# Kernel tuning notes

Measured on AMD Instinct MI355X. Metric: run time of the kernel, lower is better.

Reference implementation:

```python
import jax, jax.numpy as jnp
import numpy as np

DIM = 4096
B, S = 4, 2048


def setup_inputs() -> dict:
    key = jax.random.key(0)
    ks = jax.random.split(key, 6)
    scale = 1.0 / np.sqrt(DIM)  # nn.Linear-style init scale
    return {
        "x": jax.random.normal(ks[0], (B, S, DIM), dtype=jnp.float32),
        "W1": jax.random.normal(ks[1], (DIM, DIM), dtype=jnp.float32) * scale,
        "W2": jax.random.normal(ks[2], (DIM, DIM), dtype=jnp.float32) * scale,
        "W3": jax.random.normal(ks[3], (DIM, DIM), dtype=jnp.float32) * scale,
        "W4": jax.random.normal(ks[4], (DIM, DIM), dtype=jnp.float32) * scale,
        "Wo": jax.random.normal(ks[5], (DIM, DIM), dtype=jnp.float32) * scale,
    }


def reference(x, W1, W2, W3, W4, Wo):
    # nn.Linear(bias=False): y = x @ W.T
    xA = jnp.einsum('bsd,ed->bse', x, W1)
    xB = jnp.einsum('bsd,ed->bse', x, W2)
    xC = jnp.einsum('bsd,ed->bse', x, W3)
    # xA^T @ xB over the sequence axis -> [B, dim, dim]
    sq = jnp.einsum('bsd,bse->bde', xA, xB)
    sq = jax.nn.softmax(sq, axis=-1)
    # xC @ sq -> [B, S, dim]
    xO = jnp.einsum('bsd,bde->bse', xC, sq)
    xO = jax.nn.softmax(xO, axis=-1)
    xO = jax.nn.silu(jnp.einsum('bsd,ed->bse', xO, W4))
    return jnp.einsum('bsd,ed->bse', x + xO, Wo)
```

## Files before the change

kernel.cpp:

```cpp
#include <hip/hip_runtime.h>
#include <hip/hip_bf16.h>
#include <stdint.h>

#define DIM 4096
#define NB 4
#define SEQ 2048

typedef __bf16 bf16_t;
typedef __bf16 bf16x8 __attribute__((ext_vector_type(8)));
typedef float f32x4 __attribute__((ext_vector_type(4)));

__device__ __forceinline__ uint16_t f2bf_u(float f) {
  union { float f; uint32_t u; } v; v.f = f;
  uint32_t r = v.u + 0x7FFFu + ((v.u >> 16) & 1u);
  return (uint16_t)(r >> 16);
}
__device__ __forceinline__ float bfu2f(uint32_t u) {
  union { uint32_t u; float f; } v; v.u = u << 16; return v.f;
}

__global__ __launch_bounds__(256) void cvt_f32_bf16_k(const float* __restrict__ in,
                                                      uint16_t* __restrict__ out, long n) {
  long i = ((long)blockIdx.x * 256 + threadIdx.x) * 8;
  long stride = (long)gridDim.x * 256 * 8;
  for (; i < n; i += stride) {
    float4 a = *(const float4*)(in + i);
    float4 b = *(const float4*)(in + i + 4);
    ushort4 o0 = make_ushort4(f2bf_u(a.x), f2bf_u(a.y), f2bf_u(a.z), f2bf_u(a.w));
    ushort4 o1 = make_ushort4(f2bf_u(b.x), f2bf_u(b.y), f2bf_u(b.z), f2bf_u(b.w));
    *(ushort4*)(out + i) = o0;
    *(ushort4*)(out + i + 4) = o1;
  }
}

__device__ __forceinline__ void gload16(const void* g, void* l) {
  __builtin_amdgcn_global_load_lds(
      (const __attribute__((address_space(1))) void*)g,
      (__attribute__((address_space(3))) void*)l,
      16, 0, 0);
}

#define BARX() do { asm volatile("" ::: "memory"); __builtin_amdgcn_s_barrier(); asm volatile("" ::: "memory"); } while (0)
#define VMW(n) asm volatile("s_waitcnt vmcnt(" #n ")" ::: "memory")

__device__ __forceinline__ void readA(bf16x8 (&fa)[4][2], const char* p, int c0, int c1) {
#pragma unroll
  for (int m = 0; m < 4; ++m) {
    fa[m][0] = *(const bf16x8*)(p + m * 2048 + c0);
    fa[m][1] = *(const bf16x8*)(p + m * 2048 + c1);
  }
}
__device__ __forceinline__ void readB(bf16x8 (&fb)[2][2], const char* p, int c0, int c1) {
#pragma unroll
  for (int n = 0; n < 2; ++n) {
    fb[n][0] = *(const bf16x8*)(p + n * 2048 + c0);
    fb[n][1] = *(const bf16x8*)(p + n * 2048 + c1);
  }
}
__device__ __forceinline__ void mmaQ(f32x4 (&acc)[4][2], const bf16x8 (&fa)[4][2],
                                     const bf16x8 (&fb)[2][2]) {
#pragma unroll
  for (int m = 0; m < 4; ++m)
#pragma unroll
    for (int n = 0; n < 2; ++n)
#pragma unroll
      for (int kk = 0; kk < 2; ++kk)
        acc[m][n] = __builtin_amdgcn_mfma_f32_16x16x32_bf16(fa[m][kk], fb[n][kk], acc[m][n], 0, 0, 0);
}
__device__ __forceinline__ void stageH(const bf16_t* gt, int soff, long rsk, char* lb, int t16) {
  gload16(gt + soff, lb + t16);
  gload16(gt + soff + rsk, lb + 8192 + t16);
}

#define PRIO1() __builtin_amdgcn_s_setprio(1)
#define PRIO0() __builtin_amdgcn_s_setprio(0)

template <int EPI>
__global__ __launch_bounds__(512, 2) void gemm256(
    const bf16_t* __restrict__ Abase, const bf16_t* __restrict__ Bbase,
    void* __restrict__ Cout, const float* __restrict__ Xadd,
    int M, int N, int K, long sA, long sB, long sC) {
  __shared__ char smem[131072];
  char* As = smem;
  char* Bs = smem + 65536;

  const int tid = threadIdx.x;
  const int lane = tid & 63;
  const int wave = tid >> 6;
  const int wm = wave >> 2;
  const int wn = wave & 3;
  const int lr = lane & 15;
  const int hi = lane >> 4;

  const int nwg = gridDim.x;
  int wg = blockIdx.x;
  if ((nwg & 7) == 0) wg = (wg & 7) * (nwg >> 3) + (wg >> 3);
  const int nbn = N >> 8;
  const int bm = wg / nbn, bn = wg % nbn;

  const bf16_t* A = Abase + (long)blockIdx.y * sA;
  const bf16_t* B = Bbase + (long)blockIdx.y * sB;
  const bf16_t* A0p = A + (long)(bm * 256) * K;
  const bf16_t* A1p = A0p + (long)128 * K;
  const bf16_t* B0p = B + (long)(bn * 256) * K;
  const bf16_t* B1p = B0p + (long)128 * K;
  const long rsk = (long)64 * K;

  const int t16 = tid * 16;
  const int lp = t16 ^ (((t16 >> 7) & 7) << 4);
  const int soff = (lp >> 7) * K + ((lp & 127) >> 1);

  const int swz = (lr & 7) << 4;
  const int c0 = (hi * 16) ^ swz;
  const int c1 = c0 ^ 64;
  const int aR = (wm * 64 + lr) * 128;
  const int bR = (wn * 32 + lr) * 128;

  f32x4 acc[2][2][4][2] = {};
  bf16x8 fa0[4][2], fa1[4][2], fb0[2][2], fb1[2][2];

  stageH(A0p, soff, rsk, As, t16);
  stageH(A1p, soff, rsk, As + 16384, t16);
  stageH(B0p, soff, rsk, Bs, t16);
  stageH(B1p, soff, rsk, Bs + 16384, t16);
  VMW(4);
  stageH(A0p + 64, soff, rsk, As + 32768, t16);
  stageH(A1p + 64, soff, rsk, As + 49152, t16);
  stageH(B0p + 64, soff, rsk, Bs + 32768, t16);
  VMW(6);
  BARX();

  const int NIT = K >> 7;
  for (int i = 0; i < NIT; ++i) {
    const bool last = (i == NIT - 1);
    const int k1 = (2 * i + 1) * 64;
    readA(fa0, As + aR, c0, c1);
    readB(fb0, Bs + bR, c0, c1);
    stageH(B1p + k1, soff, rsk, Bs + 49152, t16);
    BARX();
    PRIO1(); mmaQ(acc[0][0], fa0, fb0); PRIO0();
    BARX();
    readA(fa1, As + 16384 + aR, c0, c1);
    if (!last) stageH(A0p + k1 + 64, soff, rsk, As, t16);
    BARX();
    PRIO1(); mmaQ(acc[1][0], fa1, fb0); PRIO0();
    BARX();
    readB(fb1, Bs + 16384 + bR, c0, c1);
    if (!last) stageH(A1p + k1 + 64, soff, rsk, As + 16384, t16);
    BARX();
    PRIO1(); mmaQ(acc[0][1], fa0, fb1); PRIO0();
    BARX();
    if (!last) stageH(B0p + k1 + 64, soff, rsk, Bs, t16);
    BARX();
    PRIO1(); mmaQ(acc[1][1], fa1, fb1); PRIO0();
    if (last) { VMW(0); } else { VMW(6); }
    BARX();
    readA(fa0, As + 32768 + aR, c0, c1);
    readB(fb0, Bs + 32768 + bR, c0, c1);
    if (!last) stageH(B1p + k1 + 64, soff, rsk, Bs + 16384, t16);
    BARX();
    PRIO1(); mmaQ(acc[0][0], fa0, fb0); PRIO0();
    BARX();
    readA(fa1, As + 49152 + aR, c0, c1);
    if (!last) stageH(A0p + k1 + 128, soff, rsk, As + 32768, t16);
    BARX();
    PRIO1(); mmaQ(acc[1][0], fa1, fb0); PRIO0();
    BARX();
    readB(fb1, Bs + 49152 + bR, c0, c1);
    if (!last) stageH(A1p + k1 + 128, soff, rsk, As + 49152, t16);
    BARX();
    PRIO1(); mmaQ(acc[0][1], fa0, fb1); PRIO0();
    BARX();
    if (!last) stageH(B0p + k1 + 128, soff, rsk, Bs + 32768, t16);
    BARX();
    PRIO1(); mmaQ(acc[1][1], fa1, fb1); PRIO0();
    if (!last) VMW(6);
    BARX();
  }

  const long cb = (long)blockIdx.y * sC;
#pragma unroll
  for (int mh = 0; mh < 2; ++mh)
#pragma unroll
    for (int nh = 0; nh < 2; ++nh)
#pragma unroll
      for (int m = 0; m < 4; ++m)
#pragma unroll
        for (int n = 0; n < 2; ++n)
#pragma unroll
          for (int j = 0; j < 4; ++j) {
            const int row = bm * 256 + mh * 128 + wm * 64 + m * 16 + hi * 4 + j;
            const int col = bn * 256 + nh * 128 + wn * 32 + n * 16 + lr;
            const long idx = cb + (long)row * N + col;
            const float vv = acc[mh][nh][m][n][j];
            if constexpr (EPI == 0) {
              ((uint16_t*)Cout)[idx] = f2bf_u(vv);
            } else if constexpr (EPI == 1) {
              ((float*)Cout)[idx] = vv;
            } else {
              const float sl = vv / (1.f + __expf(-vv));
              ((uint16_t*)Cout)[idx] = f2bf_u(Xadd[idx] + sl);
            }
          }
}

__global__ __launch_bounds__(256) void rowstat4096_bf16(const uint16_t* __restrict__ in,
                                                        float2* __restrict__ stats) {
  const long row = blockIdx.x;
  const uint16_t* r = in + row * 4096;
  const int tid = threadIdx.x;
  uint32_t w[8];
  *(uint4*)(w) = *(const uint4*)(r + tid * 16);
  *(uint4*)(w + 4) = *(const uint4*)(r + tid * 16 + 8);
  float v[16];
#pragma unroll
  for (int j = 0; j < 8; ++j) {
    v[2 * j] = bfu2f(w[j] & 0xFFFFu);
    v[2 * j + 1] = bfu2f(w[j] >> 16);
  }
  float m = v[0];
#pragma unroll
  for (int j = 1; j < 16; ++j) m = fmaxf(m, v[j]);
#pragma unroll
  for (int o = 32; o; o >>= 1) m = fmaxf(m, __shfl_xor(m, o));
  __shared__ float red[8];
  if ((tid & 63) == 0) red[tid >> 6] = m;
  __syncthreads();
  m = fmaxf(fmaxf(red[0], red[1]), fmaxf(red[2], red[3]));
  float s = 0.f;
#pragma unroll
  for (int j = 0; j < 16; ++j) s += __expf(v[j] - m);
#pragma unroll
  for (int o = 32; o; o >>= 1) s += __shfl_xor(s, o);
  if ((tid & 63) == 0) red[4 + (tid >> 6)] = s;
  __syncthreads();
  if (tid == 0) {
    s = (red[4] + red[5]) + (red[6] + red[7]);
    stats[row] = make_float2(m, 1.f / s);
  }
}

__global__ __launch_bounds__(256) void transposeSM_bf16(const uint16_t* __restrict__ inB,
                                                        const float2* __restrict__ statsB,
                                                        uint16_t* __restrict__ outB) {
  const int b = blockIdx.z;
  const uint16_t* in = inB + (long)b * (4096L * 4096);
  const float2* stats = statsB + (long)b * 4096;
  uint16_t* out = outB + (long)b * (4096L * 4096);
  __shared__ uint16_t t[64][68];
  __shared__ float2 st[64];
  const int tid = threadIdx.x;
  const int bx = blockIdx.x, by = blockIdx.y;
  if (tid < 64) st[tid] = stats[by * 64 + tid];
  __syncthreads();
  const int tr = tid >> 4;
  const int tc4 = (tid & 15) * 4;
#pragma unroll
  for (int i = 0; i < 4; ++i) {
    const int r = tr + i * 16;
    const float2 ms = st[r];
    ushort4 u = *(const ushort4*)&in[(long)(by * 64 + r) * 4096 + bx * 64 + tc4];
    t[r][tc4 + 0] = f2bf_u(__expf(bfu2f(u.x) - ms.x) * ms.y);
    t[r][tc4 + 1] = f2bf_u(__expf(bfu2f(u.y) - ms.x) * ms.y);
    t[r][tc4 + 2] = f2bf_u(__expf(bfu2f(u.z) - ms.x) * ms.y);
    t[r][tc4 + 3] = f2bf_u(__expf(bfu2f(u.w) - ms.x) * ms.y);
  }
  __syncthreads();
#pragma unroll
  for (int i = 0; i < 4; ++i) {
    const int oc = tr + i * 16;
    ushort4 v = make_ushort4(t[tc4 + 0][oc], t[tc4 + 1][oc], t[tc4 + 2][oc], t[tc4 + 3][oc]);
    *(ushort4*)&out[(long)(bx * 64 + oc) * 4096 + by * 64 + tc4] = v;
  }
}

__global__ __launch_bounds__(256) void softmax_row4096_bf16(const uint16_t* __restrict__ in,
                                                            uint16_t* __restrict__ out) {
  const long row = blockIdx.x;
  const uint16_t* r = in + row * 4096;
  const int tid = threadIdx.x;
  uint32_t w[8];
  *(uint4*)(w) = *(const uint4*)(r + tid * 16);
  *(uint4*)(w + 4) = *(const uint4*)(r + tid * 16 + 8);
  float v[16];
#pragma unroll
  for (int j = 0; j < 8; ++j) {
    v[2 * j] = bfu2f(w[j] & 0xFFFFu);
    v[2 * j + 1] = bfu2f(w[j] >> 16);
  }
  float m = v[0];
#pragma unroll
  for (int j = 1; j < 16; ++j) m = fmaxf(m, v[j]);
#pragma unroll
  for (int o = 32; o; o >>= 1) m = fmaxf(m, __shfl_xor(m, o));
  __shared__ float red[8];
  if ((tid & 63) == 0) red[tid >> 6] = m;
  __syncthreads();
  m = fmaxf(fmaxf(red[0], red[1]), fmaxf(red[2], red[3]));
  float s = 0.f;
#pragma unroll
  for (int j = 0; j < 16; ++j) { v[j] = __expf(v[j] - m); s += v[j]; }
#pragma unroll
  for (int o = 32; o; o >>= 1) s += __shfl_xor(s, o);
  if ((tid & 63) == 0) red[4 + (tid >> 6)] = s;
  __syncthreads();
  s = (red[4] + red[5]) + (red[6] + red[7]);
  float inv = 1.f / s;
#pragma unroll
  for (int i = 0; i < 4; ++i) {
    ushort4 u = make_ushort4(f2bf_u(v[i * 4 + 0] * inv), f2bf_u(v[i * 4 + 1] * inv),
                             f2bf_u(v[i * 4 + 2] * inv), f2bf_u(v[i * 4 + 3] * inv));
    *(ushort4*)(out + row * 4096 + tid * 16 + i * 4) = u;
  }
}

extern "C" void kernel_launch(void* const* d_in, const int* in_sizes, int n_in,
                              void* d_out, int out_size, void* d_ws, size_t ws_size,
                              hipStream_t stream) {
  const float* x  = (const float*)d_in[0];
  const float* W1 = (const float*)d_in[1];
  const float* W2 = (const float*)d_in[2];
  const float* W3 = (const float*)d_in[3];
  const float* W4 = (const float*)d_in[4];
  const float* Wo = (const float*)d_in[5];

  char* ws = (char*)d_ws;
  const long SD  = (long)SEQ * DIM;
  const long BSD = (long)NB * SD;
  const long DD  = (long)DIM * DIM;

  bf16_t* xbf  = (bf16_t*)(ws + 0L);
  bf16_t* xW   = (bf16_t*)(ws + 67108864L);
  bf16_t* R3   = (bf16_t*)(ws + 201326592L);
  bf16_t* Wbf  = (bf16_t*)(ws + 268435456L);
  bf16_t* sqmT = (bf16_t*)(ws + 301989888L);
  float2* stats = (float2*)Wbf;
  (void)ws_size; (void)in_sizes; (void)n_in; (void)out_size;

  cvt_f32_bf16_k<<<2048, 256, 0, stream>>>(x, (uint16_t*)xbf, BSD);

  cvt_f32_bf16_k<<<2048, 256, 0, stream>>>(W1, (uint16_t*)R3, DD);
  cvt_f32_bf16_k<<<2048, 256, 0, stream>>>(W2, (uint16_t*)(R3 + DD), DD);
  gemm256<0><<<dim3(256, 4), 512, 0, stream>>>(R3, xbf, (void*)xW, nullptr,
                                               2 * DIM, SEQ, DIM, 0, SD, 2 * SD);

  gemm256<0><<<dim3(256, 4), 512, 0, stream>>>(xW, xW + SD, d_out, nullptr,
                                               DIM, DIM, SEQ, 2 * SD, 2 * SD, DD);
  rowstat4096_bf16<<<NB * DIM, 256, 0, stream>>>((const uint16_t*)d_out, stats);
  transposeSM_bf16<<<dim3(64, 64, 4), 256, 0, stream>>>((const uint16_t*)d_out, stats,
                                                        (uint16_t*)sqmT);

  cvt_f32_bf16_k<<<2048, 256, 0, stream>>>(W3, (uint16_t*)Wbf, DD);
  gemm256<0><<<dim3(512, 1), 512, 0, stream>>>(xbf, Wbf, (void*)R3, nullptr,
                                               NB * SEQ, DIM, DIM, 0, 0, 0);

  gemm256<0><<<dim3(128, 4), 512, 0, stream>>>(R3, sqmT, d_out, nullptr,
                                               SEQ, DIM, DIM, SD, DD, SD);
  softmax_row4096_bf16<<<NB * SEQ, 256, 0, stream>>>((const uint16_t*)d_out, (uint16_t*)xW);

  cvt_f32_bf16_k<<<2048, 256, 0, stream>>>(W4, (uint16_t*)Wbf, DD);
  gemm256<2><<<dim3(512, 1), 512, 0, stream>>>(xW, Wbf, (void*)xbf, x,
                                               NB * SEQ, DIM, DIM, 0, 0, 0);

  cvt_f32_bf16_k<<<2048, 256, 0, stream>>>(Wo, (uint16_t*)Wbf, DD);
  gemm256<1><<<dim3(512, 1), 512, 0, stream>>>(xbf, Wbf, d_out, nullptr,
                                               NB * SEQ, DIM, DIM, 0, 0, 0);
}
```

Baseline: 1.730 ms.

## Restructure GEMM main loop into a deeper software pipeline with fewer barriers

Rewrites the 256x256 bf16 GEMM main loop so each LDS fragment read is issued one step ahead of the MFMA that consumes it. The loop now uses one barrier per quarter-step instead of two, and keeps all eight half-tiles in flight using vmcnt(10) waits. The last-iteration branches are removed by wrapping prefetch offsets with a K mask, so the final iteration issues redundant loads from the start of K. This aims to overlap LDS reads, global-to-LDS loads and MFMA more tightly. The cost is extra wasted global traffic at the tail, and correctness depends on the reordered buffer reuse and waitcnt values being right.

```diff
diff --git a/kernel.cpp b/kernel.cpp
--- a/kernel.cpp
+++ b/kernel.cpp
@@ -42,6 +42,7 @@
 
 #define BARX() do { asm volatile("" ::: "memory"); __builtin_amdgcn_s_barrier(); asm volatile("" ::: "memory"); } while (0)
 #define VMW(n) asm volatile("s_waitcnt vmcnt(" #n ")" ::: "memory")
+#define LGKM(n) asm volatile("s_waitcnt lgkmcnt(" #n ")" ::: "memory")
 
 __device__ __forceinline__ void readA(bf16x8 (&fa)[4][2], const char* p, int c0, int c1) {
 #pragma unroll
@@ -120,62 +121,61 @@
   bf16x8 fa0[4][2], fa1[4][2], fb0[2][2], fb1[2][2];
 
   stageH(A0p, soff, rsk, As, t16);
-  stageH(A1p, soff, rsk, As + 16384, t16);
   stageH(B0p, soff, rsk, Bs, t16);
   stageH(B1p, soff, rsk, Bs + 16384, t16);
-  VMW(4);
+  stageH(A1p, soff, rsk, As + 16384, t16);
   stageH(A0p + 64, soff, rsk, As + 32768, t16);
+  stageH(B0p + 64, soff, rsk, Bs + 32768, t16);
+  stageH(B1p + 64, soff, rsk, Bs + 49152, t16);
   stageH(A1p + 64, soff, rsk, As + 49152, t16);
-  stageH(B0p + 64, soff, rsk, Bs + 32768, t16);
-  VMW(6);
+  VMW(12);
   BARX();
+  readA(fa0, As + aR, c0, c1);
+  readB(fb0, Bs + bR, c0, c1);
+  LGKM(0);
+  VMW(10);
+  BARX();
 
   const int NIT = K >> 7;
+  const int kmask = K - 1;
   for (int i = 0; i < NIT; ++i) {
-    const bool last = (i == NIT - 1);
-    const int k1 = (2 * i + 1) * 64;
+    const int k2 = (128 * i + 128) & kmask;
+    const int k3 = (128 * i + 192) & kmask;
+
+    readB(fb1, Bs + 16384 + bR, c0, c1);
+    stageH(A0p + k2, soff, rsk, As, t16);
+    PRIO1(); mmaQ(acc[0][0], fa0, fb0); PRIO0();
+    VMW(10); BARX();
+    readA(fa1, As + 16384 + aR, c0, c1);
+    stageH(B0p + k2, soff, rsk, Bs, t16);
+    PRIO1(); mmaQ(acc[0][1], fa0, fb1); PRIO0();
+    VMW(10); BARX();
+    readA(fa0, As + 32768 + aR, c0, c1);
+    stageH(B1p + k2, soff, rsk, Bs + 16384, t16);
+    PRIO1(); mmaQ(acc[1][1], fa1, fb1); PRIO0();
+    VMW(10); BARX();
+    PRIO1(); mmaQ(acc[1][0], fa1, fb0); PRIO0();
+    readB(fb0, Bs + 32768 + bR, c0, c1);
+    stageH(A1p + k2, soff, rsk, As + 16384, t16);
+    LGKM(4);
+    VMW(10); BARX();
+    readB(fb1, Bs + 49152 + bR, c0, c1);
+    stageH(A0p + k3, soff, rsk, As + 32768, t16);
+    PRIO1(); mmaQ(acc[0][0], fa0, fb0); PRIO0();
+    VMW(10); BARX();
+    readA(fa1, As + 49152 + aR, c0, c1);
+    stageH(B0p + k3, soff, rsk, Bs + 32768, t16);
+    PRIO1(); mmaQ(acc[0][1], fa0, fb1); PRIO0();
+    VMW(10); BARX();
     readA(fa0, As + aR, c0, c1);
+    stageH(B1p + k3, soff, rsk, Bs + 49152, t16);
+    PRIO1(); mmaQ(acc[1][1], fa1, fb1); PRIO0();
+    VMW(10); BARX();
+    PRIO1(); mmaQ(acc[1][0], fa1, fb0); PRIO0();
     readB(fb0, Bs + bR, c0, c1);
-    stageH(B1p + k1, soff, rsk, Bs + 49152, t16);
-    BARX();
-    PRIO1(); mmaQ(acc[0][0], fa0, fb0); PRIO0();
-    BARX();
-    readA(fa1, As + 16384 + aR, c0, c1);
-    if (!last) stageH(A0p + k1 + 64, soff, rsk, As, t16);
-    BARX();
-    PRIO1(); mmaQ(acc[1][0], fa1, fb0); PRIO0();
-    BARX();
-    readB(fb1, Bs + 16384 + bR, c0, c1);
-    if (!last) stageH(A1p + k1 + 64, soff, rsk, As + 16384, t16);
-    BARX();
-    PRIO1(); mmaQ(acc[0][1], fa0, fb1); PRIO0();
-    BARX();
-    if (!last) stageH(B0p + k1 + 64, soff, rsk, Bs, t16);
-    BARX();
-    PRIO1(); mmaQ(acc[1][1], fa1, fb1); PRIO0();
-    if (last) { VMW(0); } else { VMW(6); }
-    BARX();
-    readA(fa0, As + 32768 + aR, c0, c1);
-    readB(fb0, Bs + 32768 + bR, c0, c1);
-    if (!last) stageH(B1p + k1 + 64, soff, rsk, Bs + 16384, t16);
-    BARX();
-    PRIO1(); mmaQ(acc[0][0], fa0, fb0); PRIO0();
-    BARX();
-    readA(fa1, As + 49152 + aR, c0, c1);
-    if (!last) stageH(A0p + k1 + 128, soff, rsk, As + 32768, t16);
-    BARX();
-    PRIO1(); mmaQ(acc[1][0], fa1, fb0); PRIO0();
-    BARX();
-    readB(fb1, Bs + 49152 + bR, c0, c1);
-    if (!last) stageH(A1p + k1 + 128, soff, rsk, As + 49152, t16);
-    BARX();
-    PRIO1(); mmaQ(acc[0][1], fa0, fb1); PRIO0();
-    BARX();
-    if (!last) stageH(B0p + k1 + 128, soff, rsk, Bs + 32768, t16);
-    BARX();
-    PRIO1(); mmaQ(acc[1][1], fa1, fb1); PRIO0();
-    if (!last) VMW(6);
-    BARX();
+    stageH(A1p + k3, soff, rsk, As + 49152, t16);
+    LGKM(4);
+    VMW(10); BARX();
   }
 
   const long cb = (long)blockIdx.y * sC;
```

Result: faster. 1.685 ms (-2.6%).
